# Optimization experiments

Hardware: AMD Instinct MI355X
Metric: run time of the kernel (lower is better)

## Reference

```python
import jax, jax.numpy as jnp
import numpy as np

N_HEADS = 16
ROPE_BASE = 10000.0

def _rope_cos_sin(seq_len, head_dim):
    # freqs[t, j] = t / base**(2j/head_dim), j over head_dim//2 pairs
    inv_freq = 1.0 / (ROPE_BASE ** (jnp.arange(0, head_dim, 2, dtype=jnp.float32) / head_dim))
    t = jnp.arange(seq_len, dtype=jnp.float32)
    freqs = t[:, None] * inv_freq[None, :]          # [S, hd/2]
    return jnp.cos(freqs), jnp.sin(freqs)

def _apply_rope(x, cos, sin):
    # x: [B, S, H, hd]; pairs are interleaved (even, odd) -> complex (re, im)
    xr = x[..., 0::2]
    xi = x[..., 1::2]
    c = cos[None, :, None, :]
    s = sin[None, :, None, :]
    out_r = xr * c - xi * s
    out_i = xr * s + xi * c
    # interleave back: [..., hd/2, 2] -> [..., hd]
    return jnp.stack([out_r, out_i], axis=-1).reshape(x.shape)

def setup_inputs() -> dict:
    key = jax.random.key(0)
    ks = jax.random.split(key, 5)
    B, S, D = 2, 2048, 2048
    x = jax.random.normal(ks[0], (B, S, D), dtype=jnp.float32)
    w_scale = 0.02
    wq = jax.random.normal(ks[1], (D, D), dtype=jnp.float32) * w_scale
    wk = jax.random.normal(ks[2], (D, D), dtype=jnp.float32) * w_scale
    wv = jax.random.normal(ks[3], (D, D), dtype=jnp.float32) * w_scale
    wo = jax.random.normal(ks[4], (D, D), dtype=jnp.float32) * w_scale
    return {"x": x, "wq": wq, "wk": wk, "wv": wv, "wo": wo}

def reference(x, wq, wk, wv, wo):
    B, S, D = x.shape
    H = N_HEADS
    hd = D // H
    # QKV projections (torch Linear: y = x @ W^T)
    q = (x @ wq.T).reshape(B, S, H, hd)
    k = (x @ wk.T).reshape(B, S, H, hd)
    v = (x @ wv.T).reshape(B, S, H, hd)
    cos, sin = _rope_cos_sin(S, hd)
    q = _apply_rope(q, cos, sin)
    k = _apply_rope(k, cos, sin)
    # -> [B, H, S, hd]
    q = q.transpose(0, 2, 1, 3)
    k = k.transpose(0, 2, 1, 3)
    v = v.transpose(0, 2, 1, 3)
    scale = 1.0 / jnp.sqrt(jnp.float32(hd))
    scores = jnp.einsum('bhqd,bhkd->bhqk', q, k) * scale
    causal = jnp.tril(jnp.ones((S, S), dtype=bool))
    scores = jnp.where(causal[None, None], scores, jnp.float32(-1e30))
    probs = jax.nn.softmax(scores, axis=-1)
    attn = jnp.einsum('bhqk,bhkd->bhqd', probs, v)  # [B, H, S, hd]
    attn = attn.transpose(0, 2, 1, 3).reshape(B, S, D)
    return attn @ wo.T
```

## Files before the change

### kernel.cpp

```cpp
#include <hip/hip_runtime.h>
#include <hip/hip_bf16.h>

using bf16 = __hip_bfloat16;
typedef __attribute__((ext_vector_type(8))) short short8;
typedef __attribute__((ext_vector_type(4))) float floatx4;
typedef __attribute__((ext_vector_type(2))) float floatx2;

#define GLDS16(g, l)                                                        \
  __builtin_amdgcn_global_load_lds(                                         \
      (const __attribute__((address_space(1))) void*)(g),                   \
      (__attribute__((address_space(3))) void*)(l), 16, 0, 0)

#define MFMA16(a, b, c) __builtin_amdgcn_mfma_f32_16x16x32_bf16(a, b, c, 0, 0, 0)

__device__ __forceinline__ short f2b(float x) {
  union { bf16 h; short s; } u;
  u.h = __float2bfloat16(x);
  return u.s;
}
__device__ __forceinline__ void st(float* p, float v) { *p = v; }
__device__ __forceinline__ void st(bf16* p, float v) { *p = __float2bfloat16(v); }

template <int CTRL>
__device__ __forceinline__ float dpp_f(float x) {
  return __int_as_float(__builtin_amdgcn_update_dpp(
      0, __float_as_int(x), CTRL, 0xF, 0xF, true));
}
__device__ __forceinline__ float red16_max(float x) {
  x = fmaxf(x, dpp_f<0xB1>(x));
  x = fmaxf(x, dpp_f<0x4E>(x));
  x = fmaxf(x, dpp_f<0x141>(x));
  x = fmaxf(x, dpp_f<0x140>(x));
  return x;
}
__device__ __forceinline__ float red16_sum(float x) {
  x += dpp_f<0xB1>(x);
  x += dpp_f<0x4E>(x);
  x += dpp_f<0x141>(x);
  x += dpp_f<0x140>(x);
  return x;
}

__global__ void cast_kernel(const float* __restrict__ in, bf16* __restrict__ out,
                            long n) {
  long i = ((long)blockIdx.x * blockDim.x + threadIdx.x) * 8;
  if (i >= n) return;
  floatx4 a = *(const floatx4*)(in + i);
  floatx4 b = *(const floatx4*)(in + i + 4);
  short8 r;
  r[0] = f2b(a[0]); r[1] = f2b(a[1]); r[2] = f2b(a[2]); r[3] = f2b(a[3]);
  r[4] = f2b(b[0]); r[5] = f2b(b[1]); r[6] = f2b(b[2]); r[7] = f2b(b[3]);
  *(short8*)(out + i) = r;
}

__global__ void rope_tab_kernel(floatx2* __restrict__ tab) {
  const int t = blockIdx.x * blockDim.x + threadIdx.x;
  const int s = t >> 6, p = t & 63;
  const float invf = exp2f(-(float)p * (13.287712379549449f / 64.0f));
  float sn, cs;
  sincosf((float)s * invf, &sn, &cs);
  floatx2 e; e[0] = cs; e[1] = sn;
  tab[t] = e;
}

__device__ __forceinline__ void gemm_core(
    const bf16* __restrict__ A, const bf16* __restrict__ B, int K,
    long m0, long n0, bf16* As, bf16* Bs, floatx4 (&acc)[4][4])
{
  const int tid  = threadIdx.x;
  const int wave = tid >> 6;
  const int lane = tid & 63;
  const int quad = lane >> 4;
  const int l16  = lane & 15;
  const int wr = wave >> 2;
  const int wc = wave & 3;

  const int arow = tid >> 2;
  const int acol = (tid & 3) ^ ((tid >> 3) & 3);
  const long gaoff = (m0 + arow) * (long)K + acol * 8;
  const int alds = wave * 512;
  long gb[2];
  int blds[2];
#pragma unroll
  for (int i = 0; i < 2; i++) {
    const int c = i * 512 + tid;
    const int row = c >> 2;
    const int col = (c & 3) ^ ((c >> 3) & 3);
    gb[i] = (n0 + row) * (long)K + col * 8;
    blds[i] = (i * 512 + wave * 64) * 8;
  }

  const int qs = (quad ^ ((l16 >> 1) & 3)) * 8;

#pragma unroll
  for (int mi = 0; mi < 4; mi++)
#pragma unroll
    for (int ni = 0; ni < 4; ni++) {
      floatx4 z = {0.f, 0.f, 0.f, 0.f};
      acc[mi][ni] = z;
    }

  const int NT = K >> 5;

#pragma unroll
  for (int t = 0; t < 3; t++) {
    GLDS16(A + gaoff + t * 32, As + t * 4096 + alds);
    GLDS16(B + gb[0] + t * 32, Bs + t * 8192 + blds[0]);
    GLDS16(B + gb[1] + t * 32, Bs + t * 8192 + blds[1]);
  }
  asm volatile("s_waitcnt vmcnt(6)" ::: "memory");
  __builtin_amdgcn_s_barrier();

  for (int t = 0; t < NT; t++) {
    const bf16* Ab = As + (t & 3) * 4096;
    const bf16* Bb = Bs + (t & 3) * 8192;
    const int pf = t + 3;

    short8 a[4], b[4];
#pragma unroll
    for (int mi = 0; mi < 4; mi++)
      a[mi] = *(const short8*)(Ab + (wr * 64 + mi * 16 + l16) * 32 + qs);
#pragma unroll
    for (int ni = 0; ni < 4; ni++)
      b[ni] = *(const short8*)(Bb + (wc * 64 + ni * 16 + l16) * 32 + qs);

    if (pf < NT) {
      bf16* Apf = As + (pf & 3) * 4096;
      bf16* Bpf = Bs + (pf & 3) * 8192;
      const long pfk = (long)pf * 32;
      GLDS16(A + gaoff + pfk, Apf + alds);
      GLDS16(B + gb[0] + pfk, Bpf + blds[0]);
      GLDS16(B + gb[1] + pfk, Bpf + blds[1]);
    }
    __builtin_amdgcn_s_barrier();
    asm volatile("s_waitcnt lgkmcnt(0)" ::: "memory");
    __builtin_amdgcn_sched_barrier(0);
    __builtin_amdgcn_s_setprio(1);
#pragma unroll
    for (int mi = 0; mi < 4; mi++)
#pragma unroll
      for (int ni = 0; ni < 4; ni++)
        acc[mi][ni] = MFMA16(a[mi], b[ni], acc[mi][ni]);
    __builtin_amdgcn_s_setprio(0);

    const int staged = (pf < NT) ? pf : (NT - 1);
    const int newer  = staged - t - 1;
    if (newer >= 2)       asm volatile("s_waitcnt vmcnt(6)" ::: "memory");
    else if (newer == 1)  asm volatile("s_waitcnt vmcnt(3)" ::: "memory");
    else                  asm volatile("s_waitcnt vmcnt(0)" ::: "memory");
    __builtin_amdgcn_s_barrier();
  }
}

__global__ __launch_bounds__(512, 2) void qkv_gemm(
    const bf16* __restrict__ A,
    const bf16* __restrict__ B0, const bf16* __restrict__ B1,
    const bf16* __restrict__ B2,
    bf16* __restrict__ C0, bf16* __restrict__ C1, bf16* __restrict__ Cvt,
    const floatx2* __restrict__ rtab,
    int M, int N, int K)
{
  __shared__ __align__(16) bf16 As[4 * 4096];
  __shared__ __align__(16) bf16 Bs[4 * 8192];

  const int sel = blockIdx.y >> 3;
  const long m0 = (long)blockIdx.x * 128;
  const long n0 = (long)(blockIdx.y & 7) * 256;
  const bf16* B = (sel == 0) ? B0 : ((sel == 1) ? B1 : B2);

  floatx4 acc[4][4];
  gemm_core(A, B, K, m0, n0, As, Bs, acc);

  const int tid  = threadIdx.x;
  const int wave = tid >> 6;
  const int lane = tid & 63;
  const int quad = lane >> 4;
  const int l16  = lane & 15;
  const int wr = wave >> 2;
  const int wc = wave & 3;

  if (sel < 2) {
    bf16* C = (sel == 0) ? C0 : C1;
    const float sgn = (l16 & 1) ? 1.0f : -1.0f;
#pragma unroll
    for (int ni = 0; ni < 4; ni++) {
      const int n = (int)n0 + wc * 64 + ni * 16 + l16;
      const int p = (n & 127) >> 1;
#pragma unroll
      for (int mi = 0; mi < 4; mi++) {
        floatx4 v = acc[mi][ni];
        const int mbase = (int)m0 + wr * 64 + mi * 16 + quad * 4;
#pragma unroll
        for (int r = 0; r < 4; r++) {
          const int spos = (mbase + r) & 2047;
          const floatx2 cssn = rtab[spos * 64 + p];
          const float pv = dpp_f<0xB1>(v[r]);
          const float outv = v[r] * cssn[0] + pv * (sgn * cssn[1]);
          st(&C[(long)(mbase + r) * N + n], outv);
        }
      }
    }
  } else {
#pragma unroll
    for (int ni = 0; ni < 4; ni++) {
      const int n = (int)n0 + wc * 64 + ni * 16 + l16;
      const int hh = n >> 7, d = n & 127;
#pragma unroll
      for (int mi = 0; mi < 4; mi++) {
        floatx4 v = acc[mi][ni];
        const int m = (int)m0 + wr * 64 + mi * 16 + quad * 4;
        const int bb = m >> 11, s = m & 2047;
        unsigned long long pk =
            (unsigned long long)(unsigned short)f2b(v[0]) |
            ((unsigned long long)(unsigned short)f2b(v[1]) << 16) |
            ((unsigned long long)(unsigned short)f2b(v[2]) << 32) |
            ((unsigned long long)(unsigned short)f2b(v[3]) << 48);
        *(unsigned long long*)(Cvt + ((long)((bb * 16 + hh) * 128 + d)) * 2048 + s) = pk;
      }
    }
  }
}

__global__ __launch_bounds__(512, 2) void gemm_out(
    const bf16* __restrict__ A, const bf16* __restrict__ B,
    float* __restrict__ C, int M, int N, int K)
{
  __shared__ __align__(16) bf16 As[4 * 4096];
  __shared__ __align__(16) bf16 Bs[4 * 8192];
  const long m0 = (long)blockIdx.x * 128;
  const long n0 = (long)blockIdx.y * 256;

  floatx4 acc[4][4];
  gemm_core(A, B, K, m0, n0, As, Bs, acc);

  const int tid  = threadIdx.x;
  const int wave = tid >> 6;
  const int lane = tid & 63;
  const int quad = lane >> 4;
  const int l16  = lane & 15;
  const int wr = wave >> 2;
  const int wc = wave & 3;

#pragma unroll
  for (int mi = 0; mi < 4; mi++)
#pragma unroll
    for (int ni = 0; ni < 4; ni++) {
      floatx4 v = acc[mi][ni];
      const long row = m0 + wr * 64 + mi * 16 + quad * 4;
      const long col = n0 + wc * 64 + ni * 16 + l16;
#pragma unroll
      for (int r = 0; r < 4; r++)
        C[(row + r) * (long)N + col] = v[r];
    }
}

#define NEG_BIG (-30000.0f)

__global__ __launch_bounds__(256) void flash_attn(
    const bf16* __restrict__ q, const bf16* __restrict__ k,
    const bf16* __restrict__ vt, bf16* __restrict__ o, int S)
{
  __shared__ bf16 Ks[64 * 136];
  __shared__ bf16 Vt[128 * 72];
  __shared__ bf16 Ps[4][32 * 72];

  const int tid  = threadIdx.x;
  const int wave = tid >> 6;
  const int lane = tid & 63;
  const int quad = lane >> 4;
  const int l16  = lane & 15;

  const int bh = blockIdx.x;
  const int b  = bh >> 4, h = bh & 15;
  const int q0 = ((int)gridDim.y - 1 - (int)blockIdx.y) * 128;

  const bf16* Qb = q + ((long)b * S * 16 + h) * 128;
  const bf16* Kb = k + ((long)b * S * 16 + h) * 128;
  const bf16* Vg = vt + (long)bh * 128 * S;
  bf16*       Ob = o + ((long)b * S * 16 + h) * 128;

  int kr[4], kc[4], vr[4], vc[4];
#pragma unroll
  for (int it = 0; it < 4; it++) {
    const int c = tid + it * 256;
    kr[it] = c >> 4;  kc[it] = (c & 15) * 8;
    vr[it] = c >> 3;  vc[it] = (c & 7) * 8;
  }

  short8 aq[2][4];
#pragma unroll
  for (int mi = 0; mi < 2; mi++)
#pragma unroll
    for (int kt = 0; kt < 4; kt++)
      aq[mi][kt] = *(const short8*)(
          Qb + (long)(q0 + wave * 32 + mi * 16 + l16) * 2048 + kt * 32 + quad * 8);

  float m_i[2][4], l_i[2][4];
  floatx4 oacc[2][8];
  const floatx4 zero4 = {0.f, 0.f, 0.f, 0.f};
#pragma unroll
  for (int mi = 0; mi < 2; mi++) {
#pragma unroll
    for (int r = 0; r < 4; r++) { m_i[mi][r] = NEG_BIG; l_i[mi][r] = 0.f; }
#pragma unroll
    for (int dt = 0; dt < 8; dt++) oacc[mi][dt] = zero4;
  }

  const float SCL2 = 0.08838834764831845f * 1.4426950408889634f;
  const int wrow0 = q0 + wave * 32;
  const int last  = q0 + 64;

  short8 kreg[4], vreg[4];
#pragma unroll
  for (int it = 0; it < 4; it++) {
    kreg[it] = *(const short8*)(Kb + (long)kr[it] * 2048 + kc[it]);
    vreg[it] = *(const short8*)(Vg + (long)vr[it] * S + vc[it]);
  }

  for (int kt0 = 0; kt0 <= last; kt0 += 64) {
    __syncthreads();

#pragma unroll
    for (int it = 0; it < 4; it++) {
      *(short8*)(Ks + kr[it] * 136 + kc[it]) = kreg[it];
      *(short8*)(Vt + vr[it] * 72 + vc[it]) = vreg[it];
    }
    __syncthreads();

    if (kt0 < last) {
      const int n0 = kt0 + 64;
#pragma unroll
      for (int it = 0; it < 4; it++) {
        kreg[it] = *(const short8*)(Kb + (long)(n0 + kr[it]) * 2048 + kc[it]);
        vreg[it] = *(const short8*)(Vg + (long)vr[it] * S + n0 + vc[it]);
      }
    }

    if (kt0 <= wrow0 + 31) {
      floatx4 sc[2][4];
#pragma unroll
      for (int mi = 0; mi < 2; mi++)
#pragma unroll
        for (int nt = 0; nt < 4; nt++) sc[mi][nt] = zero4;
#pragma unroll
      for (int nt = 0; nt < 4; nt++)
#pragma unroll
        for (int kt = 0; kt < 4; kt++) {
          short8 bk = *(const short8*)(Ks + (nt * 16 + l16) * 136 + kt * 32 + quad * 8);
          sc[0][nt] = __builtin_amdgcn_mfma_f32_16x16x32_bf16(aq[0][kt], bk, sc[0][nt], 0, 0, 0);
          sc[1][nt] = __builtin_amdgcn_mfma_f32_16x16x32_bf16(aq[1][kt], bk, sc[1][nt], 0, 0, 0);
        }

      const bool needmask = (kt0 + 63 > wrow0);
      float alpha[2][4];
#pragma unroll
      for (int mi = 0; mi < 2; mi++) {
#pragma unroll
        for (int r = 0; r < 4; r++) {
          const int qr = wrow0 + mi * 16 + quad * 4 + r;
          float mx = NEG_BIG;
          if (needmask) {
#pragma unroll
            for (int nt = 0; nt < 4; nt++) {
              const int kc2 = kt0 + nt * 16 + l16;
              float vsc = sc[mi][nt][r] * SCL2;
              vsc = (kc2 <= qr) ? vsc : NEG_BIG;
              sc[mi][nt][r] = vsc;
              mx = fmaxf(mx, vsc);
            }
          } else {
#pragma unroll
            for (int nt = 0; nt < 4; nt++) {
              float vsc = sc[mi][nt][r] * SCL2;
              sc[mi][nt][r] = vsc;
              mx = fmaxf(mx, vsc);
            }
          }
          mx = red16_max(mx);
          const float mnew = fmaxf(m_i[mi][r], mx);

          alpha[mi][r] = exp2f(m_i[mi][r] - mnew);
          float rs = 0.f;
#pragma unroll
          for (int nt = 0; nt < 4; nt++) {
            float p = exp2f(sc[mi][nt][r] - mnew);
            sc[mi][nt][r] = p;
            rs += p;
          }
          rs = red16_sum(rs);
          l_i[mi][r] = l_i[mi][r] * alpha[mi][r] + rs;
          m_i[mi][r] = mnew;
        }
      }

#pragma unroll
      for (int mi = 0; mi < 2; mi++)
#pragma unroll
        for (int nt = 0; nt < 4; nt++)
#pragma unroll
          for (int r = 0; r < 4; r++)
            Ps[wave][(mi * 16 + quad * 4 + r) * 72 + nt * 16 + l16] =
                __float2bfloat16(sc[mi][nt][r]);

#pragma unroll
      for (int mi = 0; mi < 2; mi++)
#pragma unroll
        for (int dt = 0; dt < 8; dt++)
#pragma unroll
          for (int r = 0; r < 4; r++)
            oacc[mi][dt][r] *= alpha[mi][r];

#pragma unroll
      for (int ks = 0; ks < 2; ks++) {
        short8 ap0 = *(const short8*)(&Ps[wave][(l16) * 72 + ks * 32 + quad * 8]);
        short8 ap1 = *(const short8*)(&Ps[wave][(16 + l16) * 72 + ks * 32 + quad * 8]);
#pragma unroll
        for (int dt = 0; dt < 8; dt++) {
          short8 bv = *(const short8*)(Vt + (dt * 16 + l16) * 72 + ks * 32 + quad * 8);
          oacc[0][dt] = __builtin_amdgcn_mfma_f32_16x16x32_bf16(ap0, bv, oacc[0][dt], 0, 0, 0);
          oacc[1][dt] = __builtin_amdgcn_mfma_f32_16x16x32_bf16(ap1, bv, oacc[1][dt], 0, 0, 0);
        }
      }
    }
  }

#pragma unroll
  for (int mi = 0; mi < 2; mi++)
#pragma unroll
    for (int r = 0; r < 4; r++) {
      const float inv = 1.0f / l_i[mi][r];
      const long s = q0 + wave * 32 + mi * 16 + quad * 4 + r;
#pragma unroll
      for (int dt = 0; dt < 8; dt++)
        Ob[s * 2048 + dt * 16 + l16] = __float2bfloat16(oacc[mi][dt][r] * inv);
    }
}

extern "C" void kernel_launch(void* const* d_in, const int* in_sizes, int n_in,
                              void* d_out, int out_size, void* d_ws, size_t ws_size,
                              hipStream_t stream) {
  const float* x  = (const float*)d_in[0];
  const float* wq = (const float*)d_in[1];
  const float* wk = (const float*)d_in[2];
  const float* wv = (const float*)d_in[3];
  const float* wo = (const float*)d_in[4];
  float* out = (float*)d_out;

  const int B = 2, S = 2048, D = 2048, H = 16;
  const int M = B * S;
  const long tsz = (long)M * D;
  const long wsz = (long)D * D;

  if (ws_size < 4 * (size_t)tsz * sizeof(bf16)) return;

  bf16* qb  = (bf16*)d_ws;
  bf16* kb  = qb + tsz;
  bf16* vtb = kb + tsz;
  bf16* ab  = vtb + tsz;

  bf16* xb  = (bf16*)d_out;
  bf16* wqb = xb + tsz;
  bf16* wkb = wqb + wsz;
  bf16* wvb = ab;
  floatx2* rtab = (floatx2*)(ab + wsz);
  bf16* wob = qb;

  cast_kernel<<<(int)(tsz / 8 / 256), 256, 0, stream>>>(x,  xb,  tsz);
  cast_kernel<<<(int)(wsz / 8 / 256), 256, 0, stream>>>(wq, wqb, wsz);
  cast_kernel<<<(int)(wsz / 8 / 256), 256, 0, stream>>>(wk, wkb, wsz);
  cast_kernel<<<(int)(wsz / 8 / 256), 256, 0, stream>>>(wv, wvb, wsz);
  rope_tab_kernel<<<(S * 64) / 256, 256, 0, stream>>>(rtab);

  qkv_gemm<<<dim3(M / 128, 24), 512, 0, stream>>>(
      xb, wqb, wkb, wvb, qb, kb, vtb, rtab, M, D, D);

  flash_attn<<<dim3(B * H, S / 128), 256, 0, stream>>>(qb, kb, vtb, ab, S);

  cast_kernel<<<(int)(wsz / 8 / 256), 256, 0, stream>>>(wo, wob, wsz);
  gemm_out<<<dim3(M / 128, D / 256), 512, 0, stream>>>(ab, wob, out, M, D, D);
}
```

Before: 425.3 us.

## Use 256x256 tiles with double-buffered K-halves for QKV GEMM

```diff
diff --git a/kernel.cpp b/kernel.cpp
--- a/kernel.cpp
+++ b/kernel.cpp
@@ -63,7 +63,144 @@
   tab[t] = e;
 }
 
-__device__ __forceinline__ void gemm_core(
+__device__ __forceinline__ void gemm_core256(
+    const bf16* __restrict__ A, const bf16* __restrict__ B, int K,
+    long m0, long n0, bf16* As, bf16* Bs, floatx4 (&acc)[8][4])
+{
+  const int tid  = threadIdx.x;
+  const int wave = tid >> 6;
+  const int lane = tid & 63;
+  const int quad = lane >> 4;
+  const int l16  = lane & 15;
+  const int wr = wave >> 2;
+  const int wc = wave & 3;
+
+  long ga[2], gb[2];
+  int soff[2];
+#pragma unroll
+  for (int i = 0; i < 2; i++) {
+    const int c = i * 512 + tid;
+    const int row = c >> 2;
+    const int gch = (c & 3) ^ ((c >> 3) & 3);
+    ga[i] = (m0 + row) * (long)K + gch * 8;
+    gb[i] = (n0 + row) * (long)K + gch * 8;
+    soff[i] = (i * 512 + wave * 64) * 8;
+  }
+
+  const int qs = (quad ^ ((l16 >> 1) & 3)) * 8;
+
+#pragma unroll
+  for (int mi = 0; mi < 8; mi++)
+#pragma unroll
+    for (int ni = 0; ni < 4; ni++) {
+      floatx4 z = {0.f, 0.f, 0.f, 0.f};
+      acc[mi][ni] = z;
+    }
+
+  const int NT = K >> 6;
+
+#pragma unroll
+  for (int kh = 0; kh < 2; kh++) {
+    GLDS16(A + ga[0] + kh * 32, As + kh * 8192 + soff[0]);
+    GLDS16(A + ga[1] + kh * 32, As + kh * 8192 + soff[1]);
+    GLDS16(B + gb[0] + kh * 32, Bs + kh * 8192 + soff[0]);
+    GLDS16(B + gb[1] + kh * 32, Bs + kh * 8192 + soff[1]);
+  }
+
+  for (int kt = 0; kt < NT; kt++) {
+    const bf16* Ab = As + (kt & 1) * 16384;
+    const bf16* Bb = Bs + (kt & 1) * 16384;
+    bf16* An = As + ((kt + 1) & 1) * 16384;
+    bf16* Bn = Bs + ((kt + 1) & 1) * 16384;
+    const long nk = (long)(kt + 1) * 64;
+    const bool pf = (kt + 1) < NT;
+
+    asm volatile("s_waitcnt vmcnt(4)" ::: "memory");
+    __builtin_amdgcn_s_barrier();
+
+    short8 a0[4], b0[4];
+#pragma unroll
+    for (int mi = 0; mi < 4; mi++)
+      a0[mi] = *(const short8*)(Ab + (wr * 128 + mi * 16 + l16) * 32 + qs);
+#pragma unroll
+    for (int ni = 0; ni < 4; ni++)
+      b0[ni] = *(const short8*)(Bb + (wc * 64 + ni * 16 + l16) * 32 + qs);
+    if (pf) {
+      GLDS16(A + ga[0] + nk, An + soff[0]);
+      GLDS16(A + ga[1] + nk, An + soff[1]);
+    }
+    asm volatile("s_waitcnt lgkmcnt(0)" ::: "memory");
+    __builtin_amdgcn_sched_barrier(0);
+    __builtin_amdgcn_s_setprio(1);
+#pragma unroll
+    for (int mi = 0; mi < 4; mi++)
+#pragma unroll
+      for (int ni = 0; ni < 4; ni++)
+        acc[mi][ni] = MFMA16(a0[mi], b0[ni], acc[mi][ni]);
+    __builtin_amdgcn_s_setprio(0);
+
+    short8 a1[4];
+#pragma unroll
+    for (int mi = 0; mi < 4; mi++)
+      a1[mi] = *(const short8*)(Ab + (wr * 128 + (mi + 4) * 16 + l16) * 32 + qs);
+    if (pf) {
+      GLDS16(B + gb[0] + nk, Bn + soff[0]);
+      GLDS16(B + gb[1] + nk, Bn + soff[1]);
+    }
+    asm volatile("s_waitcnt lgkmcnt(0)" ::: "memory");
+    __builtin_amdgcn_sched_barrier(0);
+    __builtin_amdgcn_s_setprio(1);
+#pragma unroll
+    for (int mi = 0; mi < 4; mi++)
+#pragma unroll
+      for (int ni = 0; ni < 4; ni++)
+        acc[mi + 4][ni] = MFMA16(a1[mi], b0[ni], acc[mi + 4][ni]);
+    __builtin_amdgcn_s_setprio(0);
+
+    if (pf) asm volatile("s_waitcnt vmcnt(4)" ::: "memory");
+    else    asm volatile("s_waitcnt vmcnt(0)" ::: "memory");
+    __builtin_amdgcn_s_barrier();
+
+#pragma unroll
+    for (int mi = 0; mi < 4; mi++)
+      a0[mi] = *(const short8*)(Ab + 8192 + (wr * 128 + mi * 16 + l16) * 32 + qs);
+#pragma unroll
+    for (int ni = 0; ni < 4; ni++)
+      b0[ni] = *(const short8*)(Bb + 8192 + (wc * 64 + ni * 16 + l16) * 32 + qs);
+    if (pf) {
+      GLDS16(A + ga[0] + nk + 32, An + 8192 + soff[0]);
+      GLDS16(A + ga[1] + nk + 32, An + 8192 + soff[1]);
+    }
+    asm volatile("s_waitcnt lgkmcnt(0)" ::: "memory");
+    __builtin_amdgcn_sched_barrier(0);
+    __builtin_amdgcn_s_setprio(1);
+#pragma unroll
+    for (int mi = 0; mi < 4; mi++)
+#pragma unroll
+      for (int ni = 0; ni < 4; ni++)
+        acc[mi][ni] = MFMA16(a0[mi], b0[ni], acc[mi][ni]);
+    __builtin_amdgcn_s_setprio(0);
+
+#pragma unroll
+    for (int mi = 0; mi < 4; mi++)
+      a1[mi] = *(const short8*)(Ab + 8192 + (wr * 128 + (mi + 4) * 16 + l16) * 32 + qs);
+    if (pf) {
+      GLDS16(B + gb[0] + nk + 32, Bn + 8192 + soff[0]);
+      GLDS16(B + gb[1] + nk + 32, Bn + 8192 + soff[1]);
+    }
+    asm volatile("s_waitcnt lgkmcnt(0)" ::: "memory");
+    __builtin_amdgcn_sched_barrier(0);
+    __builtin_amdgcn_s_setprio(1);
+#pragma unroll
+    for (int mi = 0; mi < 4; mi++)
+#pragma unroll
+      for (int ni = 0; ni < 4; ni++)
+        acc[mi + 4][ni] = MFMA16(a1[mi], b0[ni], acc[mi + 4][ni]);
+    __builtin_amdgcn_s_setprio(0);
+  }
+}
+
+__device__ __forceinline__ void gemm_core128(
     const bf16* __restrict__ A, const bf16* __restrict__ B, int K,
     long m0, long n0, bf16* As, bf16* Bs, floatx4 (&acc)[4][4])
 {
@@ -89,7 +226,6 @@
     gb[i] = (n0 + row) * (long)K + col * 8;
     blds[i] = (i * 512 + wave * 64) * 8;
   }
-
   const int qs = (quad ^ ((l16 >> 1) & 3)) * 8;
 
 #pragma unroll
@@ -101,7 +237,6 @@
     }
 
   const int NT = K >> 5;
-
 #pragma unroll
   for (int t = 0; t < 3; t++) {
     GLDS16(A + gaoff + t * 32, As + t * 4096 + alds);
@@ -160,16 +295,16 @@
     const floatx2* __restrict__ rtab,
     int M, int N, int K)
 {
-  __shared__ __align__(16) bf16 As[4 * 4096];
-  __shared__ __align__(16) bf16 Bs[4 * 8192];
+  __shared__ __align__(16) bf16 As[2 * 16384];
+  __shared__ __align__(16) bf16 Bs[2 * 16384];
 
   const int sel = blockIdx.y >> 3;
-  const long m0 = (long)blockIdx.x * 128;
+  const long m0 = (long)blockIdx.x * 256;
   const long n0 = (long)(blockIdx.y & 7) * 256;
   const bf16* B = (sel == 0) ? B0 : ((sel == 1) ? B1 : B2);
 
-  floatx4 acc[4][4];
-  gemm_core(A, B, K, m0, n0, As, Bs, acc);
+  floatx4 acc[8][4];
+  gemm_core256(A, B, K, m0, n0, As, Bs, acc);
 
   const int tid  = threadIdx.x;
   const int wave = tid >> 6;
@@ -187,9 +322,9 @@
       const int n = (int)n0 + wc * 64 + ni * 16 + l16;
       const int p = (n & 127) >> 1;
 #pragma unroll
-      for (int mi = 0; mi < 4; mi++) {
+      for (int mi = 0; mi < 8; mi++) {
         floatx4 v = acc[mi][ni];
-        const int mbase = (int)m0 + wr * 64 + mi * 16 + quad * 4;
+        const int mbase = (int)m0 + wr * 128 + mi * 16 + quad * 4;
 #pragma unroll
         for (int r = 0; r < 4; r++) {
           const int spos = (mbase + r) & 2047;
@@ -206,9 +341,9 @@
       const int n = (int)n0 + wc * 64 + ni * 16 + l16;
       const int hh = n >> 7, d = n & 127;
 #pragma unroll
-      for (int mi = 0; mi < 4; mi++) {
+      for (int mi = 0; mi < 8; mi++) {
         floatx4 v = acc[mi][ni];
-        const int m = (int)m0 + wr * 64 + mi * 16 + quad * 4;
+        const int m = (int)m0 + wr * 128 + mi * 16 + quad * 4;
         const int bb = m >> 11, s = m & 2047;
         unsigned long long pk =
             (unsigned long long)(unsigned short)f2b(v[0]) |
@@ -231,7 +366,7 @@
   const long n0 = (long)blockIdx.y * 256;
 
   floatx4 acc[4][4];
-  gemm_core(A, B, K, m0, n0, As, Bs, acc);
+  gemm_core128(A, B, K, m0, n0, As, Bs, acc);
 
   const int tid  = threadIdx.x;
   const int wave = tid >> 6;
@@ -471,7 +606,7 @@
   cast_kernel<<<(int)(wsz / 8 / 256), 256, 0, stream>>>(wv, wvb, wsz);
   rope_tab_kernel<<<(S * 64) / 256, 256, 0, stream>>>(rtab);
 
-  qkv_gemm<<<dim3(M / 128, 24), 512, 0, stream>>>(
+  qkv_gemm<<<dim3(M / 256, 24), 512, 0, stream>>>(
       xb, wqb, wkb, wvb, qb, kb, vtb, rtab, M, D, D);
 
   flash_attn<<<dim3(B * H, S / 128), 256, 0, stream>>>(qb, kb, vtb, ab, S);
```

Result: no change. 421.3 us (-0.9%).

## Retile GEMMs to 256x128 blocks with 4 waves and 3-stage pipeline

Applied to the files above, without the earlier changes.

```diff
diff --git a/kernel.cpp b/kernel.cpp
--- a/kernel.cpp
+++ b/kernel.cpp
@@ -65,35 +65,41 @@
 
 __device__ __forceinline__ void gemm_core(
     const bf16* __restrict__ A, const bf16* __restrict__ B, int K,
-    long m0, long n0, bf16* As, bf16* Bs, floatx4 (&acc)[4][4])
+    long m0, long n0, bf16* As, bf16* Bs, floatx4 (&acc)[8][4])
 {
   const int tid  = threadIdx.x;
   const int wave = tid >> 6;
   const int lane = tid & 63;
   const int quad = lane >> 4;
   const int l16  = lane & 15;
-  const int wr = wave >> 2;
-  const int wc = wave & 3;
-
-  const int arow = tid >> 2;
-  const int acol = (tid & 3) ^ ((tid >> 3) & 3);
-  const long gaoff = (m0 + arow) * (long)K + acol * 8;
-  const int alds = wave * 512;
+  const int wr = wave >> 1;
+  const int wc = wave & 1;
+
+  long ga[4];
+  int aoff[4];
+#pragma unroll
+  for (int i = 0; i < 4; i++) {
+    const int c = i * 256 + tid;
+    const int row = c >> 2;
+    const int gch = (c & 3) ^ ((c >> 3) & 3);
+    ga[i] = (m0 + row) * (long)K + gch * 8;
+    aoff[i] = (i * 256 + wave * 64) * 8;
+  }
   long gb[2];
-  int blds[2];
+  int boff[2];
 #pragma unroll
   for (int i = 0; i < 2; i++) {
-    const int c = i * 512 + tid;
+    const int c = i * 256 + tid;
     const int row = c >> 2;
-    const int col = (c & 3) ^ ((c >> 3) & 3);
-    gb[i] = (n0 + row) * (long)K + col * 8;
-    blds[i] = (i * 512 + wave * 64) * 8;
+    const int gch = (c & 3) ^ ((c >> 3) & 3);
+    gb[i] = (n0 + row) * (long)K + gch * 8;
+    boff[i] = (i * 256 + wave * 64) * 8;
   }
 
   const int qs = (quad ^ ((l16 >> 1) & 3)) * 8;
 
 #pragma unroll
-  for (int mi = 0; mi < 4; mi++)
+  for (int mi = 0; mi < 8; mi++)
 #pragma unroll
     for (int ni = 0; ni < 4; ni++) {
       floatx4 z = {0.f, 0.f, 0.f, 0.f};
@@ -103,56 +109,59 @@
   const int NT = K >> 5;
 
 #pragma unroll
-  for (int t = 0; t < 3; t++) {
-    GLDS16(A + gaoff + t * 32, As + t * 4096 + alds);
-    GLDS16(B + gb[0] + t * 32, Bs + t * 8192 + blds[0]);
-    GLDS16(B + gb[1] + t * 32, Bs + t * 8192 + blds[1]);
-  }
-  asm volatile("s_waitcnt vmcnt(6)" ::: "memory");
-  __builtin_amdgcn_s_barrier();
-
+  for (int t = 0; t < 2; t++) {
+    bf16* Ad = As + t * 8192;
+    bf16* Bd = Bs + t * 4096;
+    const long kk = (long)t * 32;
+#pragma unroll
+    for (int i = 0; i < 4; i++) GLDS16(A + ga[i] + kk, Ad + aoff[i]);
+#pragma unroll
+    for (int i = 0; i < 2; i++) GLDS16(B + gb[i] + kk, Bd + boff[i]);
+  }
+
+  int sl = 0;
   for (int t = 0; t < NT; t++) {
-    const bf16* Ab = As + (t & 3) * 4096;
-    const bf16* Bb = Bs + (t & 3) * 8192;
-    const int pf = t + 3;
-
-    short8 a[4], b[4];
-#pragma unroll
-    for (int mi = 0; mi < 4; mi++)
-      a[mi] = *(const short8*)(Ab + (wr * 64 + mi * 16 + l16) * 32 + qs);
+    if (t < NT - 1) asm volatile("s_waitcnt vmcnt(6)" ::: "memory");
+    else            asm volatile("s_waitcnt vmcnt(0)" ::: "memory");
+    __builtin_amdgcn_s_barrier();
+
+    const bf16* Ab = As + sl * 8192;
+    const bf16* Bb = Bs + sl * 4096;
+
+    short8 a[8], b[4];
+#pragma unroll
+    for (int mi = 0; mi < 8; mi++)
+      a[mi] = *(const short8*)(Ab + (wr * 128 + mi * 16 + l16) * 32 + qs);
 #pragma unroll
     for (int ni = 0; ni < 4; ni++)
       b[ni] = *(const short8*)(Bb + (wc * 64 + ni * 16 + l16) * 32 + qs);
 
-    if (pf < NT) {
-      bf16* Apf = As + (pf & 3) * 4096;
-      bf16* Bpf = Bs + (pf & 3) * 8192;
-      const long pfk = (long)pf * 32;
-      GLDS16(A + gaoff + pfk, Apf + alds);
-      GLDS16(B + gb[0] + pfk, Bpf + blds[0]);
-      GLDS16(B + gb[1] + pfk, Bpf + blds[1]);
-    }
-    __builtin_amdgcn_s_barrier();
+    if (t + 2 < NT) {
+      int s2 = sl + 2; if (s2 >= 3) s2 -= 3;
+      bf16* Ad = As + s2 * 8192;
+      bf16* Bd = Bs + s2 * 4096;
+      const long kk = (long)(t + 2) * 32;
+#pragma unroll
+      for (int i = 0; i < 4; i++) GLDS16(A + ga[i] + kk, Ad + aoff[i]);
+#pragma unroll
+      for (int i = 0; i < 2; i++) GLDS16(B + gb[i] + kk, Bd + boff[i]);
+    }
+
     asm volatile("s_waitcnt lgkmcnt(0)" ::: "memory");
     __builtin_amdgcn_sched_barrier(0);
     __builtin_amdgcn_s_setprio(1);
 #pragma unroll
-    for (int mi = 0; mi < 4; mi++)
+    for (int mi = 0; mi < 8; mi++)
 #pragma unroll
       for (int ni = 0; ni < 4; ni++)
         acc[mi][ni] = MFMA16(a[mi], b[ni], acc[mi][ni]);
     __builtin_amdgcn_s_setprio(0);
 
-    const int staged = (pf < NT) ? pf : (NT - 1);
-    const int newer  = staged - t - 1;
-    if (newer >= 2)       asm volatile("s_waitcnt vmcnt(6)" ::: "memory");
-    else if (newer == 1)  asm volatile("s_waitcnt vmcnt(3)" ::: "memory");
-    else                  asm volatile("s_waitcnt vmcnt(0)" ::: "memory");
-    __builtin_amdgcn_s_barrier();
-  }
-}
-
-__global__ __launch_bounds__(512, 2) void qkv_gemm(
+    sl++; if (sl >= 3) sl = 0;
+  }
+}
+
+__global__ __launch_bounds__(256, 2) void qkv_gemm(
     const bf16* __restrict__ A,
     const bf16* __restrict__ B0, const bf16* __restrict__ B1,
     const bf16* __restrict__ B2,
@@ -160,15 +169,15 @@
     const floatx2* __restrict__ rtab,
     int M, int N, int K)
 {
-  __shared__ __align__(16) bf16 As[4 * 4096];
-  __shared__ __align__(16) bf16 Bs[4 * 8192];
-
-  const int sel = blockIdx.y >> 3;
-  const long m0 = (long)blockIdx.x * 128;
-  const long n0 = (long)(blockIdx.y & 7) * 256;
+  __shared__ __align__(16) bf16 As[3 * 8192];
+  __shared__ __align__(16) bf16 Bs[3 * 4096];
+
+  const int sel = blockIdx.y >> 4;
+  const long m0 = (long)blockIdx.x * 256;
+  const long n0 = (long)(blockIdx.y & 15) * 128;
   const bf16* B = (sel == 0) ? B0 : ((sel == 1) ? B1 : B2);
 
-  floatx4 acc[4][4];
+  floatx4 acc[8][4];
   gemm_core(A, B, K, m0, n0, As, Bs, acc);
 
   const int tid  = threadIdx.x;
@@ -176,8 +185,8 @@
   const int lane = tid & 63;
   const int quad = lane >> 4;
   const int l16  = lane & 15;
-  const int wr = wave >> 2;
-  const int wc = wave & 3;
+  const int wr = wave >> 1;
+  const int wc = wave & 1;
 
   if (sel < 2) {
     bf16* C = (sel == 0) ? C0 : C1;
@@ -187,9 +196,9 @@
       const int n = (int)n0 + wc * 64 + ni * 16 + l16;
       const int p = (n & 127) >> 1;
 #pragma unroll
-      for (int mi = 0; mi < 4; mi++) {
+      for (int mi = 0; mi < 8; mi++) {
         floatx4 v = acc[mi][ni];
-        const int mbase = (int)m0 + wr * 64 + mi * 16 + quad * 4;
+        const int mbase = (int)m0 + wr * 128 + mi * 16 + quad * 4;
 #pragma unroll
         for (int r = 0; r < 4; r++) {
           const int spos = (mbase + r) & 2047;
@@ -206,9 +215,9 @@
       const int n = (int)n0 + wc * 64 + ni * 16 + l16;
       const int hh = n >> 7, d = n & 127;
 #pragma unroll
-      for (int mi = 0; mi < 4; mi++) {
+      for (int mi = 0; mi < 8; mi++) {
         floatx4 v = acc[mi][ni];
-        const int m = (int)m0 + wr * 64 + mi * 16 + quad * 4;
+        const int m = (int)m0 + wr * 128 + mi * 16 + quad * 4;
         const int bb = m >> 11, s = m & 2047;
         unsigned long long pk =
             (unsigned long long)(unsigned short)f2b(v[0]) |
@@ -221,16 +230,16 @@
   }
 }
 
-__global__ __launch_bounds__(512, 2) void gemm_out(
+__global__ __launch_bounds__(256, 2) void gemm_out(
     const bf16* __restrict__ A, const bf16* __restrict__ B,
     float* __restrict__ C, int M, int N, int K)
 {
-  __shared__ __align__(16) bf16 As[4 * 4096];
-  __shared__ __align__(16) bf16 Bs[4 * 8192];
-  const long m0 = (long)blockIdx.x * 128;
-  const long n0 = (long)blockIdx.y * 256;
-
-  floatx4 acc[4][4];
+  __shared__ __align__(16) bf16 As[3 * 8192];
+  __shared__ __align__(16) bf16 Bs[3 * 4096];
+  const long m0 = (long)blockIdx.x * 256;
+  const long n0 = (long)blockIdx.y * 128;
+
+  floatx4 acc[8][4];
   gemm_core(A, B, K, m0, n0, As, Bs, acc);
 
   const int tid  = threadIdx.x;
@@ -238,15 +247,15 @@
   const int lane = tid & 63;
   const int quad = lane >> 4;
   const int l16  = lane & 15;
-  const int wr = wave >> 2;
-  const int wc = wave & 3;
-
-#pragma unroll
-  for (int mi = 0; mi < 4; mi++)
+  const int wr = wave >> 1;
+  const int wc = wave & 1;
+
+#pragma unroll
+  for (int mi = 0; mi < 8; mi++)
 #pragma unroll
     for (int ni = 0; ni < 4; ni++) {
       floatx4 v = acc[mi][ni];
-      const long row = m0 + wr * 64 + mi * 16 + quad * 4;
+      const long row = m0 + wr * 128 + mi * 16 + quad * 4;
       const long col = n0 + wc * 64 + ni * 16 + l16;
 #pragma unroll
       for (int r = 0; r < 4; r++)
@@ -471,11 +480,11 @@
   cast_kernel<<<(int)(wsz / 8 / 256), 256, 0, stream>>>(wv, wvb, wsz);
   rope_tab_kernel<<<(S * 64) / 256, 256, 0, stream>>>(rtab);
 
-  qkv_gemm<<<dim3(M / 128, 24), 512, 0, stream>>>(
+  qkv_gemm<<<dim3(16, 48), 256, 0, stream>>>(
       xb, wqb, wkb, wvb, qb, kb, vtb, rtab, M, D, D);
 
   flash_attn<<<dim3(B * H, S / 128), 256, 0, stream>>>(qb, kb, vtb, ab, S);
 
   cast_kernel<<<(int)(wsz / 8 / 256), 256, 0, stream>>>(wo, wob, wsz);
-  gemm_out<<<dim3(M / 128, D / 256), 512, 0, stream>>>(ab, wob, out, M, D, D);
-}
+  gemm_out<<<dim3(16, 16), 256, 0, stream>>>(ab, wob, out, M, D, D);
+}
```

Result: faster. 412.5 us (-3.0%).
